# Performance work log

Measured on AMD Instinct MI355X. Metric: run time of the kernel, lower is better.

## Reference

```python
import jax, jax.numpy as jnp
import numpy as np
import math

E = 256      # emb_size
H = 4        # num_heads
D = E // H   # head_dim
EXPLORE_SCALE = 0.5
EXPLOIT_SCALE = 0.5
TEMP_MIN = 0.5
TEMP_MAX = 2.0


def setup_inputs() -> dict:
    key = jax.random.key(0)
    ks = jax.random.split(key, 12)
    B, S = 4, 2048
    his_emb = jax.random.normal(ks[0], (B, S, E), dtype=jnp.float32)
    src_key_padding_mask = jax.random.randint(ks[1], (B, S), 0, 2) > 0
    explore = jax.random.uniform(ks[2], (B, S), dtype=jnp.float32)
    exploit = jax.random.uniform(ks[3], (B, S), dtype=jnp.float32)
    scale = 1.0 / math.sqrt(E)
    Wq = jax.random.normal(ks[4], (E, E), dtype=jnp.float32) * scale
    bq = jnp.zeros((E,), dtype=jnp.float32)
    Wk = jax.random.normal(ks[5], (E, E), dtype=jnp.float32) * scale
    bk = jnp.zeros((E,), dtype=jnp.float32)
    Wv = jax.random.normal(ks[6], (E, E), dtype=jnp.float32) * scale
    bv = jnp.zeros((E,), dtype=jnp.float32)
    Wo = jax.random.normal(ks[7], (E, E), dtype=jnp.float32) * scale
    bo = jnp.zeros((E,), dtype=jnp.float32)
    return {"his_emb": his_emb, "src_key_padding_mask": src_key_padding_mask,
            "explore": explore, "exploit": exploit,
            "Wq": Wq, "bq": bq, "Wk": Wk, "bk": bk,
            "Wv": Wv, "bv": bv, "Wo": Wo, "bo": bo}


def reference(his_emb, src_key_padding_mask, explore, exploit,
              Wq, bq, Wk, bk, Wv, bv, Wo, bo):
    B, S, _ = his_emb.shape
    # projections -> [B, H, S, D]
    q = (his_emb @ Wq + bq).reshape(B, S, H, D).transpose(0, 2, 1, 3)
    k = (his_emb @ Wk + bk).reshape(B, S, H, D).transpose(0, 2, 1, 3)
    v = (his_emb @ Wv + bv).reshape(B, S, H, D).transpose(0, 2, 1, 3)
    logits = jnp.einsum('bhqd,bhkd->bhqk', q, k) / math.sqrt(D)
    attn_mask = src_key_padding_mask[:, None, None, :]  # [B,1,1,S] over keys
    logits = jnp.where(attn_mask, -1e16, logits)
    # per-query dynamic temperature
    temp = 1.0 + EXPLORE_SCALE * explore - EXPLOIT_SCALE * exploit  # [B,S]
    temp = jnp.clip(temp, TEMP_MIN, TEMP_MAX)
    temp = jnp.where(src_key_padding_mask, 1.0, temp)
    logits = logits / temp[:, None, :, None]
    probs = jax.nn.softmax(logits, axis=-1)
    probs = jnp.where(attn_mask, 0.0, probs)
    probs = probs / jnp.maximum(probs.sum(axis=-1, keepdims=True), 1e-8)
    out = jnp.einsum('bhqk,bhkd->bhqd', probs, v)
    out = out.transpose(0, 2, 1, 3).reshape(B, S, E)
    out = out @ Wo + bo
    return jnp.where(src_key_padding_mask[:, :, None], 0.0, out)
```

## Files before the change

kernel.cpp:

```cpp
#include <hip/hip_runtime.h>
#include <math.h>

#define B_ 4
#define S_ 2048
#define E_ 256
#define H_ 4
#define D_ 64
#define NROW (B_*S_)
#define NCH 4
#define CHK (S_/NCH)
#define NT (CHK/64)
#define LOG2E 1.4426950408889634f
#define NFM  (-17.312340490667562f)

typedef __attribute__((ext_vector_type(8)))  short short8;
typedef __attribute__((ext_vector_type(4)))  float floatx4;
typedef __attribute__((ext_vector_type(16))) float floatx16;

__device__ __forceinline__ short f2bf(float f){
    union{float f; unsigned u;} x; x.f = f;
    unsigned r = x.u + 0x7fffu + ((x.u>>16)&1u);
    return (short)(r>>16);
}
__device__ __forceinline__ unsigned cvtpk(float a, float b){
    unsigned r; asm("v_cvt_pk_bf16_f32 %0, %1, %2" : "=v"(r) : "v"(a), "v"(b)); return r;
}

__global__ __launch_bounds__(256) void prep_w(
    const float* __restrict__ W0, const float* __restrict__ W1,
    const float* __restrict__ W2, const float* __restrict__ W3,
    short* __restrict__ T0, short* __restrict__ T1,
    short* __restrict__ T2, short* __restrict__ T3)
{
    const float* W = blockIdx.y==0?W0: blockIdx.y==1?W1: blockIdx.y==2?W2:W3;
    short*       T = blockIdx.y==0?T0: blockIdx.y==1?T1: blockIdx.y==2?T2:T3;
    __shared__ float L[64][65];
    const int t = threadIdx.x;
    const int k0 = (blockIdx.x>>2)*64, n0 = (blockIdx.x&3)*64;
    {
        int r = t>>2, c0 = (t&3)*16;
        const float4* p = (const float4*)(W + (size_t)(k0+r)*E_ + n0 + c0);
        #pragma unroll
        for (int j=0;j<4;++j){
            float4 u = p[j];
            L[r][c0+4*j]=u.x; L[r][c0+4*j+1]=u.y; L[r][c0+4*j+2]=u.z; L[r][c0+4*j+3]=u.w;
        }
    }
    __syncthreads();
    {
        int n = t>>2, kk0 = (t&3)*16;
        short8 o0, o1;
        #pragma unroll
        for(int j=0;j<8;++j) o0[j] = f2bf(L[kk0+j][n]);
        #pragma unroll
        for(int j=0;j<8;++j) o1[j] = f2bf(L[kk0+8+j][n]);
        short* dst = T + (size_t)(n0+n)*E_ + k0 + kk0;
        *(short8*)dst = o0; *(short8*)(dst+8) = o1;
    }
}

__global__ __launch_bounds__(256) void qkv_gemm(
    const float* __restrict__ X,
    const short* __restrict__ Wtq, const float* __restrict__ bq,
    const short* __restrict__ Wtk, const float* __restrict__ bk,
    const short* __restrict__ Wtv, const float* __restrict__ bv,
    short* __restrict__ Q, short* __restrict__ K, short* __restrict__ Vt)
{
    const int z = blockIdx.z;
    const short* Wt   = z==0?Wtq: z==1?Wtk:Wtv;
    const float* bias = z==0?bq:  z==1?bk:bv;

    __shared__ __align__(16) short As[64][72];
    __shared__ __align__(16) short Bs[64][72];

    const int t=threadIdx.x, w=t>>6, lane=t&63, ln=lane&15, quad=lane>>4;
    const int m0 = blockIdx.y*64, n0 = blockIdx.x*64;

    floatx4 acc[4] = {};
    for (int kt=0; kt<E_; kt+=64){
        __syncthreads();
        {
            int r=t>>2, c0=(t&3)*16;
            const float4* pa = (const float4*)(X + (size_t)(m0+r)*E_ + kt + c0);
            short8 s0, s1;
            float4 u;
            u=pa[0]; s0[0]=f2bf(u.x); s0[1]=f2bf(u.y); s0[2]=f2bf(u.z); s0[3]=f2bf(u.w);
            u=pa[1]; s0[4]=f2bf(u.x); s0[5]=f2bf(u.y); s0[6]=f2bf(u.z); s0[7]=f2bf(u.w);
            u=pa[2]; s1[0]=f2bf(u.x); s1[1]=f2bf(u.y); s1[2]=f2bf(u.z); s1[3]=f2bf(u.w);
            u=pa[3]; s1[4]=f2bf(u.x); s1[5]=f2bf(u.y); s1[6]=f2bf(u.z); s1[7]=f2bf(u.w);
            *(short8*)&As[r][c0] = s0; *(short8*)&As[r][c0+8] = s1;
            const uint4* pb = (const uint4*)(Wt + (size_t)(n0+r)*E_ + kt + c0);
            *(uint4*)&Bs[r][c0] = pb[0]; *(uint4*)&Bs[r][c0+8] = pb[1];
        }
        __syncthreads();
        short8 a0 = *(const short8*)&As[w*16+ln][quad*8];
        short8 a1 = *(const short8*)&As[w*16+ln][32+quad*8];
        #pragma unroll
        for (int c=0;c<4;++c){
            short8 b0 = *(const short8*)&Bs[c*16+ln][quad*8];
            short8 b1 = *(const short8*)&Bs[c*16+ln][32+quad*8];
            acc[c] = __builtin_amdgcn_mfma_f32_16x16x32_bf16(a0,b0,acc[c],0,0,0);
            acc[c] = __builtin_amdgcn_mfma_f32_16x16x32_bf16(a1,b1,acc[c],0,0,0);
        }
    }
    if (z<2){
        short* dst = z==0?Q:K;
        #pragma unroll
        for(int c=0;c<4;++c){
            int colg = n0 + c*16 + ln;
            float bia = bias[colg];
            #pragma unroll
            for(int reg=0;reg<4;++reg){
                int row = m0 + w*16 + quad*4 + reg;
                dst[(size_t)row*E_ + colg] = f2bf(acc[c][reg] + bia);
            }
        }
    } else {
        #pragma unroll
        for(int c=0;c<4;++c){
            int colg = n0 + c*16 + ln;
            int hx = colg>>6, d = colg&63;
            float bia = bias[colg];
            #pragma unroll
            for(int reg=0;reg<4;++reg){
                int row = m0 + w*16 + quad*4 + reg;
                int bb = row>>11, s = row&(S_-1);
                Vt[((size_t)((bb*H_+hx)*D_+d))*S_ + s] = f2bf(acc[c][reg] + bia);
            }
        }
    }
}

__global__ __launch_bounds__(256) void attn_mfma(
    const short* __restrict__ Qb, const short* __restrict__ Kb, const short* __restrict__ Vtb,
    const int* __restrict__ mask,
    const float* __restrict__ explore, const float* __restrict__ exploit,
    float* __restrict__ OP, float* __restrict__ Lb)
{
    const int bid = blockIdx.x + 16*blockIdx.y + 16*NCH*blockIdx.z;
    const int swz = (bid & 7)*128 + (bid >> 3);
    const int bx = swz & 15;
    const int ck = (swz >> 4) & (NCH-1);
    const int z  = swz >> 6;
    const int b = z >> 2, h = z & 3;
    const int q0 = bx*128;
    const int k0 = ck*CHK;

    const int t = threadIdx.x, w = t>>6, lane = t&63, l31 = lane&31, hi = lane>>5;

    __shared__ __align__(16) short Ks[2][64][72];
    __shared__ __align__(16) short Vs[2][64][72];
    __shared__ float mb[2][64];

    const int qbase = q0 + w*32;
    const int qg = qbase + l31;
    float tsc2;
    {
        float ex = explore[b*S_+qg], xp = exploit[b*S_+qg];
        float tmp = fminf(fmaxf(1.0f + 0.5f*ex - 0.5f*xp, 0.5f), 2.0f);
        if (mask[b*S_+qg]) tmp = 1.0f;
        tsc2 = LOG2E/(tmp*8.0f);
    }
    const size_t qrow = (size_t)(b*S_+qg)*E_ + h*D_ + hi*8;
    const short8 qf0 = *(const short8*)(Qb + qrow);
    const short8 qf1 = *(const short8*)(Qb + qrow + 16);
    const short8 qf2 = *(const short8*)(Qb + qrow + 32);
    const short8 qf3 = *(const short8*)(Qb + qrow + 48);

    floatx16 ofa = {}, ofb = {};
    float lacc = 0.0f;

    const int sr = t>>2, sc = (t&3)*16;
    const short* kgp = Kb  + (size_t)(b*S_)*E_ + h*D_ + sc;
    const short* vgp = Vtb + ((size_t)(b*H_+h)*D_ + sr)*S_;

    uint4 rk0, rk1, rv0, rv1; float mfv = 0.0f;
    {
        const uint4* gk = (const uint4*)(kgp + (size_t)(k0+sr)*E_);
        rk0 = gk[0]; rk1 = gk[1];
        const uint4* gv = (const uint4*)(vgp + k0 + sc);
        rv0 = gv[0]; rv1 = gv[1];
        if (t < 64) mfv = mask[b*S_ + k0 + t] ? -1e30f : NFM;
    }
    *(uint4*)&Ks[0][sr][sc] = rk0; *(uint4*)&Ks[0][sr][sc+8] = rk1;
    *(uint4*)&Vs[0][sr][sc] = rv0; *(uint4*)&Vs[0][sr][sc+8] = rv1;
    if (t < 64) mb[0][t] = mfv;
    {
        const uint4* gk = (const uint4*)(kgp + (size_t)(k0+64+sr)*E_);
        rk0 = gk[0]; rk1 = gk[1];
        const uint4* gv = (const uint4*)(vgp + k0 + 64 + sc);
        rv0 = gv[0]; rv1 = gv[1];
        if (t < 64) mfv = mask[b*S_ + k0 + 64 + t] ? -1e30f : NFM;
    }
    __syncthreads();

    int cur = 0;
    #pragma unroll 1
    for (int it = 0; it < NT; ++it){
        const short (*Kc)[72] = Ks[cur];
        const short (*Vc)[72] = Vs[cur];
        #pragma unroll
        for (int kg = 0; kg < 2; ++kg){
            floatx16 st = {};
            const short8 kf0 = *(const short8*)&Kc[kg*32+l31][hi*8];
            const short8 kf1 = *(const short8*)&Kc[kg*32+l31][16+hi*8];
            const short8 kf2 = *(const short8*)&Kc[kg*32+l31][32+hi*8];
            const short8 kf3 = *(const short8*)&Kc[kg*32+l31][48+hi*8];
            __builtin_amdgcn_s_setprio(1);
            st = __builtin_amdgcn_mfma_f32_32x32x16_bf16(kf0, qf0, st, 0,0,0);
            st = __builtin_amdgcn_mfma_f32_32x32x16_bf16(kf1, qf1, st, 0,0,0);
            st = __builtin_amdgcn_mfma_f32_32x32x16_bf16(kf2, qf2, st, 0,0,0);
            st = __builtin_amdgcn_mfma_f32_32x32x16_bf16(kf3, qf3, st, 0,0,0);
            __builtin_amdgcn_s_setprio(0);
            const float4 m0_ = *(const float4*)&mb[cur][kg*32 +      4*hi];
            const float4 m1_ = *(const float4*)&mb[cur][kg*32 +  8 + 4*hi];
            const float4 m2_ = *(const float4*)&mb[cur][kg*32 + 16 + 4*hi];
            const float4 m3_ = *(const float4*)&mb[cur][kg*32 + 24 + 4*hi];
            const float mbf[16] = {m0_.x,m0_.y,m0_.z,m0_.w, m1_.x,m1_.y,m1_.z,m1_.w,
                                   m2_.x,m2_.y,m2_.z,m2_.w, m3_.x,m3_.y,m3_.z,m3_.w};
            float pr[16];
            #pragma unroll
            for (int r = 0; r < 16; ++r){
                pr[r] = __builtin_amdgcn_exp2f(st[r]*tsc2 + mbf[r]);
                lacc += pr[r];
            }
            #pragma unroll
            for (int c = 0; c < 2; ++c){
                unsigned u0 = cvtpk(pr[c*8+0], pr[c*8+1]);
                unsigned u1 = cvtpk(pr[c*8+2], pr[c*8+3]);
                unsigned u2 = cvtpk(pr[c*8+4], pr[c*8+5]);
                unsigned u3 = cvtpk(pr[c*8+6], pr[c*8+7]);
                asm("v_permlane32_swap_b32 %0, %1" : "+v"(u0), "+v"(u2));
                asm("v_permlane32_swap_b32 %0, %1" : "+v"(u1), "+v"(u3));
                union { uint4 u; short8 s; } pc;
                pc.u.x = u0; pc.u.y = u1; pc.u.z = u2; pc.u.w = u3;
                const short8 vf0 = *(const short8*)&Vc[l31]   [kg*32 + c*16 + hi*8];
                const short8 vf1 = *(const short8*)&Vc[32+l31][kg*32 + c*16 + hi*8];
                __builtin_amdgcn_s_setprio(1);
                ofa = __builtin_amdgcn_mfma_f32_32x32x16_bf16(pc.s, vf0, ofa, 0,0,0);
                ofb = __builtin_amdgcn_mfma_f32_32x32x16_bf16(pc.s, vf1, ofb, 0,0,0);
                __builtin_amdgcn_s_setprio(0);
            }
        }
        if (it + 1 < NT){
            *(uint4*)&Ks[cur^1][sr][sc] = rk0; *(uint4*)&Ks[cur^1][sr][sc+8] = rk1;
            *(uint4*)&Vs[cur^1][sr][sc] = rv0; *(uint4*)&Vs[cur^1][sr][sc+8] = rv1;
            if (t < 64) mb[cur^1][t] = mfv;
            if (it + 2 < NT){
                const int kt2 = k0 + (it+2)*64;
                const uint4* gk = (const uint4*)(kgp + (size_t)(kt2+sr)*E_);
                rk0 = gk[0]; rk1 = gk[1];
                const uint4* gv = (const uint4*)(vgp + kt2 + sc);
                rv0 = gv[0]; rv1 = gv[1];
                if (t < 64) mfv = mask[b*S_ + kt2 + t] ? -1e30f : NFM;
            }
        }
        __syncthreads();
        cur ^= 1;
    }

    const float l = lacc + __shfl_xor(lacc, 32);
    const size_t obase = ((size_t)(ck*B_+b)*H_+h)*S_;
    if (hi == 0) Lb[obase + qg] = l;
    #pragma unroll
    for (int r = 0; r < 16; ++r){
        const int q = qbase + (r&3) + 8*(r>>2) + 4*hi;
        float* dst = OP + (obase + q)*D_;
        dst[l31]      = ofa[r];
        dst[32 + l31] = ofb[r];
    }
}

__global__ __launch_bounds__(256) void out_gemm(
    const float* __restrict__ OP, const float* __restrict__ Lb,
    const short* __restrict__ Wto, const float* __restrict__ bo,
    const int* __restrict__ mask, float* __restrict__ out)
{
    __shared__ __align__(16) short As[64][72];
    __shared__ __align__(16) short Bs[64][72];
    const int bid = blockIdx.x + 4*blockIdx.y;
    const int swz = (bid & 7)*64 + (bid >> 3);
    const int n0 = (swz & 3)*64;
    const int m0 = (swz >> 2)*64;
    const int t=threadIdx.x, w=t>>6, lane=t&63, ln=lane&15, quad=lane>>4;
    floatx4 acc[4] = {};
    const int sr=t>>2, sc=(t&3)*16;
    const int rowg = m0 + sr, bb = rowg>>11, ss = rowg&(S_-1);
    #pragma unroll 1
    for (int kt=0; kt<E_; kt+=64){
        const int hx = kt>>6;
        float lsum = 0.0f;
        float4 A0={0,0,0,0}, A1={0,0,0,0}, A2={0,0,0,0}, A3={0,0,0,0};
        #pragma unroll
        for (int c=0;c<NCH;++c){
            const size_t rr = ((size_t)(c*B_+bb)*H_+hx)*S_+ss;
            lsum += Lb[rr];
            const float* pa = OP + rr*D_ + sc;
            const float4 x0=*(const float4*)(pa+0), x1=*(const float4*)(pa+4),
                         x2=*(const float4*)(pa+8), x3=*(const float4*)(pa+12);
            A0.x+=x0.x; A0.y+=x0.y; A0.z+=x0.z; A0.w+=x0.w;
            A1.x+=x1.x; A1.y+=x1.y; A1.z+=x1.z; A1.w+=x1.w;
            A2.x+=x2.x; A2.y+=x2.y; A2.z+=x2.z; A2.w+=x2.w;
            A3.x+=x3.x; A3.y+=x3.y; A3.z+=x3.z; A3.w+=x3.w;
        }
        const float rl = 1.0f/fmaxf(lsum, 1e-8f);
        const uint4* pb = (const uint4*)(Wto + (size_t)(n0+sr)*E_ + kt + sc);
        const uint4 bw0 = pb[0], bw1 = pb[1];
        __syncthreads();
        union { uint4 u; short8 s; } cA, cB;
        cA.u.x = cvtpk(A0.x*rl, A0.y*rl);
        cA.u.y = cvtpk(A0.z*rl, A0.w*rl);
        cA.u.z = cvtpk(A1.x*rl, A1.y*rl);
        cA.u.w = cvtpk(A1.z*rl, A1.w*rl);
        cB.u.x = cvtpk(A2.x*rl, A2.y*rl);
        cB.u.y = cvtpk(A2.z*rl, A2.w*rl);
        cB.u.z = cvtpk(A3.x*rl, A3.y*rl);
        cB.u.w = cvtpk(A3.z*rl, A3.w*rl);
        *(short8*)&As[sr][sc]   = cA.s;
        *(short8*)&As[sr][sc+8] = cB.s;
        *(uint4*)&Bs[sr][sc] = bw0; *(uint4*)&Bs[sr][sc+8] = bw1;
        __syncthreads();
        const short8 a0 = *(const short8*)&As[w*16+ln][quad*8];
        const short8 a1 = *(const short8*)&As[w*16+ln][32+quad*8];
        #pragma unroll
        for (int c=0;c<4;++c){
            const short8 b0 = *(const short8*)&Bs[c*16+ln][quad*8];
            const short8 b1 = *(const short8*)&Bs[c*16+ln][32+quad*8];
            acc[c] = __builtin_amdgcn_mfma_f32_16x16x32_bf16(a0,b0,acc[c],0,0,0);
            acc[c] = __builtin_amdgcn_mfma_f32_16x16x32_bf16(a1,b1,acc[c],0,0,0);
        }
    }
    #pragma unroll
    for(int c=0;c<4;++c){
        const int colg = n0 + c*16 + ln;
        const float bia = bo[colg];
        #pragma unroll
        for(int reg=0;reg<4;++reg){
            const int row = m0 + w*16 + quad*4 + reg;
            out[(size_t)row*E_ + colg] = mask[row] ? 0.0f : (acc[c][reg] + bia);
        }
    }
}

extern "C" void kernel_launch(void* const* d_in, const int* in_sizes, int n_in,
                              void* d_out, int out_size, void* d_ws, size_t ws_size,
                              hipStream_t stream) {
    const float* his     = (const float*)d_in[0];
    const int*   mask    = (const int*)d_in[1];
    const float* explore = (const float*)d_in[2];
    const float* exploit = (const float*)d_in[3];
    const float* Wq = (const float*)d_in[4];
    const float* bq = (const float*)d_in[5];
    const float* Wk = (const float*)d_in[6];
    const float* bk = (const float*)d_in[7];
    const float* Wv = (const float*)d_in[8];
    const float* bv = (const float*)d_in[9];
    const float* Wo = (const float*)d_in[10];
    const float* bo = (const float*)d_in[11];

    char* ws = (char*)d_ws;
    const size_t NE2 = (size_t)NROW * E_ * 2;
    short* Wtq  = (short*)(ws);                    ws += E_*E_*2;
    short* Wtk  = (short*)(ws);                    ws += E_*E_*2;
    short* Wtv  = (short*)(ws);                    ws += E_*E_*2;
    short* Wto  = (short*)(ws);                    ws += E_*E_*2;
    short* Qb   = (short*)(ws);                    ws += NE2;
    short* Kb   = (short*)(ws);                    ws += NE2;
    short* Vtb  = (short*)(ws);                    ws += NE2;
    float* OP   = (float*)(ws);                    ws += (size_t)NCH*NROW*E_*4;
    float* Lb   = (float*)(ws);                    ws += (size_t)NCH*B_*H_*S_*4;

    prep_w<<<dim3(16,4), 256, 0, stream>>>(Wq, Wk, Wv, Wo, Wtq, Wtk, Wtv, Wto);

    qkv_gemm<<<dim3(E_/64, NROW/64, 3), 256, 0, stream>>>(
        his, Wtq, bq, Wtk, bk, Wtv, bv, Qb, Kb, Vtb);

    attn_mfma<<<dim3(S_/128, NCH, B_*H_), 256, 0, stream>>>(
        Qb, Kb, Vtb, mask, explore, exploit, OP, Lb);

    out_gemm<<<dim3(E_/64, NROW/64), 256, 0, stream>>>(OP, Lb, Wto, bo, mask, (float*)d_out);
}
```

Before: 143.2 us.

## Fuse QKV projections into one block pass and halve attention key-split chunks

Each qkv_gemm block now loads the activation tile once and multiplies it against all three weight matrices. This removes the triple re-read and bf16 conversion of X across a z-grid dimension, and the grid is swizzled for locality. The attention split-K count drops from 4 to 2, which halves the partial-output traffic that out_gemm must reduce, but also halves the number of attention blocks. Register pressure in qkv_gemm grows with three accumulator sets, and the attention grid drops to 512 blocks, which may reduce occupancy.

```diff
diff --git a/kernel.cpp b/kernel.cpp
--- a/kernel.cpp
+++ b/kernel.cpp
@@ -7,7 +7,7 @@
 #define H_ 4
 #define D_ 64
 #define NROW (B_*S_)
-#define NCH 4
+#define NCH 2
 #define CHK (S_/NCH)
 #define NT (CHK/64)
 #define LOG2E 1.4426950408889634f
@@ -66,67 +66,67 @@
     const short* __restrict__ Wtv, const float* __restrict__ bv,
     short* __restrict__ Q, short* __restrict__ K, short* __restrict__ Vt)
 {
-    const int z = blockIdx.z;
-    const short* Wt   = z==0?Wtq: z==1?Wtk:Wtv;
-    const float* bias = z==0?bq:  z==1?bk:bv;
-
     __shared__ __align__(16) short As[64][72];
-    __shared__ __align__(16) short Bs[64][72];
+    __shared__ __align__(16) short Bs[3][64][72];
 
     const int t=threadIdx.x, w=t>>6, lane=t&63, ln=lane&15, quad=lane>>4;
-    const int m0 = blockIdx.y*64, n0 = blockIdx.x*64;
-
-    floatx4 acc[4] = {};
+    const int bid = blockIdx.x + 4*blockIdx.y;
+    const int swz = (bid & 7)*64 + (bid >> 3);
+    const int n0 = (swz & 3)*64;
+    const int m0 = (swz >> 2)*64;
+
+    floatx4 acc0[4] = {}, acc1[4] = {}, acc2[4] = {};
+    const int sr=t>>2, sc=(t&3)*16;
+    #pragma unroll 1
     for (int kt=0; kt<E_; kt+=64){
         __syncthreads();
         {
-            int r=t>>2, c0=(t&3)*16;
-            const float4* pa = (const float4*)(X + (size_t)(m0+r)*E_ + kt + c0);
-            short8 s0, s1;
-            float4 u;
+            const float4* pa = (const float4*)(X + (size_t)(m0+sr)*E_ + kt + sc);
+            short8 s0, s1; float4 u;
             u=pa[0]; s0[0]=f2bf(u.x); s0[1]=f2bf(u.y); s0[2]=f2bf(u.z); s0[3]=f2bf(u.w);
             u=pa[1]; s0[4]=f2bf(u.x); s0[5]=f2bf(u.y); s0[6]=f2bf(u.z); s0[7]=f2bf(u.w);
             u=pa[2]; s1[0]=f2bf(u.x); s1[1]=f2bf(u.y); s1[2]=f2bf(u.z); s1[3]=f2bf(u.w);
             u=pa[3]; s1[4]=f2bf(u.x); s1[5]=f2bf(u.y); s1[6]=f2bf(u.z); s1[7]=f2bf(u.w);
-            *(short8*)&As[r][c0] = s0; *(short8*)&As[r][c0+8] = s1;
-            const uint4* pb = (const uint4*)(Wt + (size_t)(n0+r)*E_ + kt + c0);
-            *(uint4*)&Bs[r][c0] = pb[0]; *(uint4*)&Bs[r][c0+8] = pb[1];
-        }
-        __syncthreads();
-        short8 a0 = *(const short8*)&As[w*16+ln][quad*8];
-        short8 a1 = *(const short8*)&As[w*16+ln][32+quad*8];
+            *(short8*)&As[sr][sc] = s0; *(short8*)&As[sr][sc+8] = s1;
+            const size_t wo = (size_t)(n0+sr)*E_ + kt + sc;
+            const uint4* pq = (const uint4*)(Wtq + wo);
+            const uint4* pk = (const uint4*)(Wtk + wo);
+            const uint4* pv = (const uint4*)(Wtv + wo);
+            *(uint4*)&Bs[0][sr][sc] = pq[0]; *(uint4*)&Bs[0][sr][sc+8] = pq[1];
+            *(uint4*)&Bs[1][sr][sc] = pk[0]; *(uint4*)&Bs[1][sr][sc+8] = pk[1];
+            *(uint4*)&Bs[2][sr][sc] = pv[0]; *(uint4*)&Bs[2][sr][sc+8] = pv[1];
+        }
+        __syncthreads();
+        const short8 a0 = *(const short8*)&As[w*16+ln][quad*8];
+        const short8 a1 = *(const short8*)&As[w*16+ln][32+quad*8];
         #pragma unroll
         for (int c=0;c<4;++c){
-            short8 b0 = *(const short8*)&Bs[c*16+ln][quad*8];
-            short8 b1 = *(const short8*)&Bs[c*16+ln][32+quad*8];
-            acc[c] = __builtin_amdgcn_mfma_f32_16x16x32_bf16(a0,b0,acc[c],0,0,0);
-            acc[c] = __builtin_amdgcn_mfma_f32_16x16x32_bf16(a1,b1,acc[c],0,0,0);
-        }
-    }
-    if (z<2){
-        short* dst = z==0?Q:K;
-        #pragma unroll
-        for(int c=0;c<4;++c){
-            int colg = n0 + c*16 + ln;
-            float bia = bias[colg];
-            #pragma unroll
-            for(int reg=0;reg<4;++reg){
-                int row = m0 + w*16 + quad*4 + reg;
-                dst[(size_t)row*E_ + colg] = f2bf(acc[c][reg] + bia);
-            }
-        }
-    } else {
-        #pragma unroll
-        for(int c=0;c<4;++c){
-            int colg = n0 + c*16 + ln;
-            int hx = colg>>6, d = colg&63;
-            float bia = bias[colg];
-            #pragma unroll
-            for(int reg=0;reg<4;++reg){
-                int row = m0 + w*16 + quad*4 + reg;
-                int bb = row>>11, s = row&(S_-1);
-                Vt[((size_t)((bb*H_+hx)*D_+d))*S_ + s] = f2bf(acc[c][reg] + bia);
-            }
+            short8 b0 = *(const short8*)&Bs[0][c*16+ln][quad*8];
+            short8 b1 = *(const short8*)&Bs[0][c*16+ln][32+quad*8];
+            acc0[c] = __builtin_amdgcn_mfma_f32_16x16x32_bf16(a0,b0,acc0[c],0,0,0);
+            acc0[c] = __builtin_amdgcn_mfma_f32_16x16x32_bf16(a1,b1,acc0[c],0,0,0);
+            b0 = *(const short8*)&Bs[1][c*16+ln][quad*8];
+            b1 = *(const short8*)&Bs[1][c*16+ln][32+quad*8];
+            acc1[c] = __builtin_amdgcn_mfma_f32_16x16x32_bf16(a0,b0,acc1[c],0,0,0);
+            acc1[c] = __builtin_amdgcn_mfma_f32_16x16x32_bf16(a1,b1,acc1[c],0,0,0);
+            b0 = *(const short8*)&Bs[2][c*16+ln][quad*8];
+            b1 = *(const short8*)&Bs[2][c*16+ln][32+quad*8];
+            acc2[c] = __builtin_amdgcn_mfma_f32_16x16x32_bf16(a0,b0,acc2[c],0,0,0);
+            acc2[c] = __builtin_amdgcn_mfma_f32_16x16x32_bf16(a1,b1,acc2[c],0,0,0);
+        }
+    }
+    #pragma unroll
+    for(int c=0;c<4;++c){
+        const int colg = n0 + c*16 + ln;
+        const float bq_ = bq[colg], bk_ = bk[colg], bv_ = bv[colg];
+        const int hx = colg>>6, d = colg&63;
+        #pragma unroll
+        for(int reg=0;reg<4;++reg){
+            const int row = m0 + w*16 + quad*4 + reg;
+            Q[(size_t)row*E_ + colg] = f2bf(acc0[c][reg] + bq_);
+            K[(size_t)row*E_ + colg] = f2bf(acc1[c][reg] + bk_);
+            const int bb = row>>11, s = row&(S_-1);
+            Vt[((size_t)((bb*H_+hx)*D_+d))*S_ + s] = f2bf(acc2[c][reg] + bv_);
         }
     }
 }
@@ -138,10 +138,10 @@
     float* __restrict__ OP, float* __restrict__ Lb)
 {
     const int bid = blockIdx.x + 16*blockIdx.y + 16*NCH*blockIdx.z;
-    const int swz = (bid & 7)*128 + (bid >> 3);
+    const int swz = (bid & 7)*64 + (bid >> 3);
     const int bx = swz & 15;
     const int ck = (swz >> 4) & (NCH-1);
-    const int z  = swz >> 6;
+    const int z  = swz >> 5;
     const int b = z >> 2, h = z & 3;
     const int q0 = bx*128;
     const int k0 = ck*CHK;
@@ -289,33 +289,28 @@
     #pragma unroll 1
     for (int kt=0; kt<E_; kt+=64){
         const int hx = kt>>6;
-        float lsum = 0.0f;
-        float4 A0={0,0,0,0}, A1={0,0,0,0}, A2={0,0,0,0}, A3={0,0,0,0};
-        #pragma unroll
-        for (int c=0;c<NCH;++c){
-            const size_t rr = ((size_t)(c*B_+bb)*H_+hx)*S_+ss;
-            lsum += Lb[rr];
-            const float* pa = OP + rr*D_ + sc;
-            const float4 x0=*(const float4*)(pa+0), x1=*(const float4*)(pa+4),
-                         x2=*(const float4*)(pa+8), x3=*(const float4*)(pa+12);
-            A0.x+=x0.x; A0.y+=x0.y; A0.z+=x0.z; A0.w+=x0.w;
-            A1.x+=x1.x; A1.y+=x1.y; A1.z+=x1.z; A1.w+=x1.w;
-            A2.x+=x2.x; A2.y+=x2.y; A2.z+=x2.z; A2.w+=x2.w;
-            A3.x+=x3.x; A3.y+=x3.y; A3.z+=x3.z; A3.w+=x3.w;
-        }
+        const size_t r0 = ((size_t)(bb)*H_+hx)*S_+ss;
+        const size_t r1 = ((size_t)(B_+bb)*H_+hx)*S_+ss;
+        const float lsum = Lb[r0] + Lb[r1];
         const float rl = 1.0f/fmaxf(lsum, 1e-8f);
+        const float* pa0 = OP + r0*D_ + sc;
+        const float* pa1 = OP + r1*D_ + sc;
+        const float4 u0 = *(const float4*)(pa0+0), u1 = *(const float4*)(pa0+4),
+                     u2 = *(const float4*)(pa0+8), u3 = *(const float4*)(pa0+12);
+        const float4 v0 = *(const float4*)(pa1+0), v1 = *(const float4*)(pa1+4),
+                     v2 = *(const float4*)(pa1+8), v3 = *(const float4*)(pa1+12);
         const uint4* pb = (const uint4*)(Wto + (size_t)(n0+sr)*E_ + kt + sc);
         const uint4 bw0 = pb[0], bw1 = pb[1];
         __syncthreads();
         union { uint4 u; short8 s; } cA, cB;
-        cA.u.x = cvtpk(A0.x*rl, A0.y*rl);
-        cA.u.y = cvtpk(A0.z*rl, A0.w*rl);
-        cA.u.z = cvtpk(A1.x*rl, A1.y*rl);
-        cA.u.w = cvtpk(A1.z*rl, A1.w*rl);
-        cB.u.x = cvtpk(A2.x*rl, A2.y*rl);
-        cB.u.y = cvtpk(A2.z*rl, A2.w*rl);
-        cB.u.z = cvtpk(A3.x*rl, A3.y*rl);
-        cB.u.w = cvtpk(A3.z*rl, A3.w*rl);
+        cA.u.x = cvtpk((u0.x+v0.x)*rl, (u0.y+v0.y)*rl);
+        cA.u.y = cvtpk((u0.z+v0.z)*rl, (u0.w+v0.w)*rl);
+        cA.u.z = cvtpk((u1.x+v1.x)*rl, (u1.y+v1.y)*rl);
+        cA.u.w = cvtpk((u1.z+v1.z)*rl, (u1.w+v1.w)*rl);
+        cB.u.x = cvtpk((u2.x+v2.x)*rl, (u2.y+v2.y)*rl);
+        cB.u.y = cvtpk((u2.z+v2.z)*rl, (u2.w+v2.w)*rl);
+        cB.u.z = cvtpk((u3.x+v3.x)*rl, (u3.y+v3.y)*rl);
+        cB.u.w = cvtpk((u3.z+v3.z)*rl, (u3.w+v3.w)*rl);
         *(short8*)&As[sr][sc]   = cA.s;
         *(short8*)&As[sr][sc+8] = cB.s;
         *(uint4*)&Bs[sr][sc] = bw0; *(uint4*)&Bs[sr][sc+8] = bw1;
@@ -372,7 +367,7 @@
 
     prep_w<<<dim3(16,4), 256, 0, stream>>>(Wq, Wk, Wv, Wo, Wtq, Wtk, Wtv, Wto);
 
-    qkv_gemm<<<dim3(E_/64, NROW/64, 3), 256, 0, stream>>>(
+    qkv_gemm<<<dim3(4, NROW/64), 256, 0, stream>>>(
         his, Wtq, bq, Wtk, bk, Wtv, bv, Qb, Kb, Vtb);
 
     attn_mfma<<<dim3(S_/128, NCH, B_*H_), 256, 0, stream>>>(
```

Result: faster. 134.4 us (-6.1%).
